# Performance work log

Measured on AMD Instinct MI355X. Metric: run time of the kernel, lower is better.

The kernel has to match this reference:

```python
import jax, jax.numpy as jnp
import numpy as np

T, B, D, H = 512, 256, 256, 256


def setup_inputs() -> dict:
    key = jax.random.key(0)
    ks = jax.random.split(key, 8)
    x = jax.random.normal(ks[0], (T, B, D), dtype=jnp.float32)
    h0 = jax.random.normal(ks[1], (1, B, H), dtype=jnp.float32)
    c0 = jax.random.normal(ks[2], (1, B, H), dtype=jnp.float32)
    W_ih = jax.random.normal(ks[3], (4 * H, D), dtype=jnp.float32) / np.sqrt(D)
    W_hh = jax.random.normal(ks[4], (4 * H, H), dtype=jnp.float32) / np.sqrt(H)
    b_ih = jnp.zeros((4 * H,), dtype=jnp.float32)
    b_hh = jnp.zeros((4 * H,), dtype=jnp.float32)
    done = jax.random.randint(ks[5], (T, B), 0, 2, dtype=jnp.int32)
    return {"x": x, "h0": h0, "c0": c0, "W_ih": W_ih, "W_hh": W_hh,
            "b_ih": b_ih, "b_hh": b_hh, "done": done}


def reference(x, h0, c0, W_ih, W_hh, b_ih, b_hh, done):
    done_f = done.astype(x.dtype)  # [T, B]
    # Precompute input contribution to gates for all timesteps: [T, B, 4H]
    gx = jnp.einsum('tbd,gd->tbg', x, W_ih) + b_ih + b_hh

    def step(carry, inp):
        h, c = carry                      # [B, H] each
        gxt, dt = inp                     # [B, 4H], [B]
        mask = (1.0 - dt)[:, None]        # reset hidden state where done
        h = h * mask
        c = c * mask
        gates = gxt + jnp.einsum('bh,gh->bg', h, W_hh)  # [B, 4H]
        i, f, g, o = jnp.split(gates, 4, axis=-1)       # PyTorch LSTM gate order
        c = jax.nn.sigmoid(f) * c + jax.nn.sigmoid(i) * jnp.tanh(g)
        h = jax.nn.sigmoid(o) * jnp.tanh(c)
        return (h, c), h

    (hT, cT), feats = jax.lax.scan(step, (h0[0], c0[0]), (gx, done_f))
    rnn_feature = feats.reshape(T * B, H)
    return rnn_feature, hT[None], cT[None]
```

## Files before the change

kernel.cpp:

```cpp
#include <hip/hip_runtime.h>
#include <math.h>

#define T_DIM 512
#define B_DIM 256
#define D_DIM 256
#define H_DIM 256
#define G_DIM 1024
#define K_DIM 512
#define NROUNDS 40
#define CHAIN_K 16

typedef __attribute__((ext_vector_type(8))) short short8;
typedef __attribute__((ext_vector_type(4))) float f32x4;

__device__ __forceinline__ unsigned int f2bf(float f) {
    unsigned int b = __float_as_uint(f);
    return (b + 0x7FFFu + ((b >> 16) & 1u)) >> 16;
}
__device__ __forceinline__ unsigned long long pack4(float4 v) {
    const unsigned int lo = (f2bf(v.y) << 16) | f2bf(v.x);
    const unsigned int hi = (f2bf(v.w) << 16) | f2bf(v.z);
    return ((unsigned long long)hi << 32) | lo;
}
__device__ __forceinline__ float sigm(float x) { return 1.0f / (1.0f + __expf(-x)); }
__device__ __forceinline__ float tanh_fast(float x) { return 2.0f / (1.0f + __expf(-2.0f * x)) - 1.0f; }

__device__ __forceinline__ void dma16(const void* g, void* l) {
    __builtin_amdgcn_global_load_lds(
        (const __attribute__((address_space(1))) void*)g,
        (__attribute__((address_space(3))) void*)l, 16, 0, 0);
}

__global__ __launch_bounds__(256) void k_prep_weights(
    const float* __restrict__ W_ih, const float* __restrict__ W_hh,
    const float* __restrict__ b_ih, const float* __restrict__ b_hh,
    unsigned int* __restrict__ Wb, float* __restrict__ bias)
{
    const int idx = blockIdx.x * 256 + threadIdx.x;
    const int jp = idx & 3, l = (idx >> 2) & 63, ks = (idx >> 8) & 15, nt = idx >> 12;
    const int g = nt * 16 + (l & 15);
    const int k0 = ks * 32 + ((l >> 4) << 3) + 2 * jp;
    const float w0 = (k0 < D_DIM) ? W_ih[g * D_DIM + k0] : W_hh[g * H_DIM + (k0 - D_DIM)];
    const float w1 = (k0 + 1 < D_DIM) ? W_ih[g * D_DIM + k0 + 1] : W_hh[g * H_DIM + (k0 + 1 - D_DIM)];
    Wb[idx] = (f2bf(w1) << 16) | f2bf(w0);
    if (idx < G_DIM) bias[idx] = b_ih[idx] + b_hh[idx];
}

__global__ __launch_bounds__(256) void k_prep_wq(
    const float* __restrict__ W_ih, const float* __restrict__ W_hh,
    unsigned long long* __restrict__ Wq)
{
    const int idx = blockIdx.x * 256 + threadIdx.x;
    const int kq = idx >> 10, g = idx & (G_DIM - 1);
    float w[4];
    #pragma unroll
    for (int j = 0; j < 4; ++j) {
        const int k = kq * 4 + j;
        w[j] = (k < D_DIM) ? W_ih[g * D_DIM + k] : W_hh[g * H_DIM + (k - D_DIM)];
    }
    Wq[idx] = pack4((float4){w[0], w[1], w[2], w[3]});
}

__global__ __launch_bounds__(256) void k_prep_ab(
    const float* __restrict__ x, unsigned long long* __restrict__ ab_u64)
{
    const int idx = blockIdx.x * 256 + threadIdx.x;
    const int pos = idx >> 6, ch = idx & 63;
    if (ch >= 32) return;
    const float4 v0 = *(const float4*)(x + (size_t)pos * D_DIM + ch * 8);
    const float4 v1 = *(const float4*)(x + (size_t)pos * D_DIM + ch * 8 + 4);
    ab_u64[(size_t)pos * 128 + ch * 2]     = pack4(v0);
    ab_u64[(size_t)pos * 128 + ch * 2 + 1] = pack4(v1);
}

__global__ __launch_bounds__(256) void k_prefill(
    const float* __restrict__ h0, const int* __restrict__ done,
    unsigned long long* __restrict__ ab_u64)
{
    const int idx = blockIdx.x * 256 + threadIdx.x;
    const int pos = idx >> 5, ch = idx & 31;
    const int d = done[pos];
    if (!d && pos >= B_DIM) return;
    unsigned long long v0 = 0ull, v1 = 0ull;
    if (!d) {
        const float4 a = *(const float4*)(h0 + (size_t)(pos & (B_DIM - 1)) * H_DIM + ch * 8);
        const float4 b = *(const float4*)(h0 + (size_t)(pos & (B_DIM - 1)) * H_DIM + ch * 8 + 4);
        v0 = pack4(a); v1 = pack4(b);
    }
    ab_u64[(size_t)pos * 128 + 64 + ch * 2]     = v0;
    ab_u64[(size_t)pos * 128 + 64 + ch * 2 + 1] = v1;
}

__global__ __launch_bounds__(256) void k_kmap(
    const int* __restrict__ done, int* __restrict__ kmap, int* __restrict__ counts)
{
    __shared__ int lcnt[NROUNDS];
    const int tid = threadIdx.x;
    if (tid < NROUNDS) lcnt[tid] = 0;
    __syncthreads();
    const int t = blockIdx.x, b = tid;
    int kv = t;
    for (int tt = t; tt >= 0; --tt) {
        if (done[tt * B_DIM + b]) { kv = t - tt; break; }
    }
    kmap[t * B_DIM + b] = kv;
    const int bin = kv < NROUNDS ? kv : NROUNDS - 1;
    atomicAdd(&lcnt[bin], 1);
    __syncthreads();
    if (tid < NROUNDS && lcnt[tid] > 0) atomicAdd(&counts[tid], lcnt[tid]);
}

__global__ __launch_bounds__(64) void k_offs(
    const int* __restrict__ counts, int* __restrict__ offs, int* __restrict__ cursor)
{
    if (threadIdx.x == 0) {
        int s = 0;
        for (int i = 0; i < NROUNDS; ++i) { offs[i] = s; s += counts[i]; }
    }
    if (threadIdx.x < NROUNDS) cursor[threadIdx.x] = 0;
}

__global__ __launch_bounds__(256) void k_scatter(
    const int* __restrict__ kmap, const int* __restrict__ offs,
    int* __restrict__ cursor, int* __restrict__ rowlist)
{
    __shared__ int lcnt[NROUNDS];
    __shared__ int gbase[NROUNDS];
    const int tid = threadIdx.x;
    if (tid < NROUNDS) lcnt[tid] = 0;
    __syncthreads();
    const int pos = blockIdx.x * 256 + tid;
    const int kv0 = kmap[pos];
    const int kv = kv0 < NROUNDS ? kv0 : NROUNDS - 1;
    const int lrank = atomicAdd(&lcnt[kv], 1);
    __syncthreads();
    if (tid < NROUNDS && lcnt[tid] > 0) gbase[tid] = atomicAdd(&cursor[tid], lcnt[tid]);
    __syncthreads();
    rowlist[offs[kv] + gbase[kv] + lrank] = pos;
}

__global__ __launch_bounds__(512, 1) void k_round(
    const short* __restrict__ ab, const float* __restrict__ c0,
    const int* __restrict__ done,
    const short* __restrict__ Wb, const float* __restrict__ bias,
    const int* __restrict__ counts, const int* __restrict__ offs,
    const int* __restrict__ rowlist,
    float* __restrict__ out, float* __restrict__ c_buf,
    short* __restrict__ ab_w, int kk)
{
    __shared__ short A_lds[2 * 32 * 512];
    __shared__ float scr[4 * 64 * 36];
    const int nk = counts[kk];
    const int base = offs[kk];
    const int ntiles = (nk + 31) >> 5;

    int cb, rt, rstride;
    if (gridDim.x == 256) {
        const int xcd = blockIdx.x & 7, slot = blockIdx.x >> 3;
        cb = slot & 3;
        rt = xcd * 8 + (slot >> 2);
        rstride = 64;
    } else {
        cb = blockIdx.x & 3;
        rt = blockIdx.x >> 2;
        rstride = gridDim.x >> 2;
    }
    if (rt >= ntiles) return;

    const int tid = threadIdx.x;
    const int w = tid >> 6, l = tid & 63;
    const int lr = l >> 4, lc = l & 15;
    const int q = w & 3, gth = w >> 2;

    const int u_ep = cb * 64 + l;
    const float bI = bias[u_ep], bF = bias[256 + u_ep], bG = bias[512 + u_ep], bO = bias[768 + u_ep];

#define ISSUE_A(PP, bufv)                                                        \
    {                                                                            \
        _Pragma("unroll") for (int rr = 0; rr < 4; ++rr) {                       \
            const int r_ = w * 4 + rr;                                           \
            dma16(ab + (size_t)PP[rr] * 512 + ((l ^ (r_ & 15)) << 3),            \
                  &A_lds[(bufv) * 16384 + r_ * 512]);                            \
        }                                                                        \
    }
#define LOAD_NEXT(row0v, PP, CP, DN, DS)                                         \
    {                                                                            \
        _Pragma("unroll") for (int j_ = 0; j_ < 4; ++j_) {                       \
            const int gr_ = (row0v) + w * 4 + j_;                                \
            PP[j_] = rowlist[base + (gr_ < nk ? gr_ : nk - 1)];                  \
        }                                                                        \
        _Pragma("unroll") for (int j_ = 0; j_ < 4; ++j_) {                       \
            const int p_ = PP[j_];                                               \
            if (kk > 0) {                                                        \
                CP[j_] = c_buf[(size_t)(p_ - B_DIM) * H_DIM + u_ep];             \
                DN[j_] = 0;                                                      \
            } else {                                                             \
                DN[j_] = done[p_];                                               \
                CP[j_] = c0[(size_t)(p_ & (B_DIM - 1)) * H_DIM + u_ep];          \
            }                                                                    \
            const int sp_ = p_ + B_DIM;                                          \
            DS[j_] = (sp_ < T_DIM * B_DIM) ? done[sp_] : 1;                      \
        }                                                                        \
    }

    int posC[4], dnC[4], dsC[4]; float cpC[4];
    LOAD_NEXT(rt * 32, posC, cpC, dnC, dsC);
    ISSUE_A(posC, 0);
    short8 breg0[16], breg1[16];
    {
        const int nt0 = (2 * gth + 0) * 16 + cb * 4 + q;
        const int nt1 = (2 * gth + 1) * 16 + cb * 4 + q;
        #pragma unroll
        for (int ks = 0; ks < 16; ++ks) {
            breg0[ks] = *(const short8*)(Wb + (((size_t)nt0 * 16 + ks) * 64 + l) * 8);
            breg1[ks] = *(const short8*)(Wb + (((size_t)nt1 * 16 + ks) * 64 + l) * 8);
        }
    }

    int buf = 0;
    for (; rt < ntiles; rt += rstride) {
        const int row0 = rt * 32;

        asm volatile("s_waitcnt vmcnt(0) lgkmcnt(0)" ::: "memory");
        __builtin_amdgcn_sched_barrier(0);
        __builtin_amdgcn_s_barrier();
        __builtin_amdgcn_sched_barrier(0);
        const int rtn = rt + rstride;
        const bool more = (rtn < ntiles);
        int posN[4], dnN[4], dsN[4]; float cpN[4];
        if (more) {
            LOAD_NEXT(rtn * 32, posN, cpN, dnN, dsN);
            ISSUE_A(posN, buf ^ 1);
        }

        f32x4 acc0[2], acc1[2];
        #pragma unroll
        for (int mb = 0; mb < 2; ++mb) { acc0[mb] = (f32x4){0,0,0,0}; acc1[mb] = (f32x4){0,0,0,0}; }
        #pragma unroll
        for (int ks = 0; ks < 16; ++ks) {
            #pragma unroll
            for (int mb = 0; mb < 2; ++mb) {
                const short8 a = *(const short8*)&A_lds[buf * 16384 + (mb * 16 + lc) * 512
                                                       + (((ks * 4 + lr) ^ lc) << 3)];
                acc0[mb] = __builtin_amdgcn_mfma_f32_16x16x32_bf16(a, breg0[ks], acc0[mb], 0, 0, 0);
                acc1[mb] = __builtin_amdgcn_mfma_f32_16x16x32_bf16(a, breg1[ks], acc1[mb], 0, 0, 0);
            }
        }

        #pragma unroll
        for (int mb = 0; mb < 2; ++mb) {
            *(f32x4*)&scr[(((2 * gth + 0) * 64 + q * 16 + lc) * 36) + mb * 16 + lr * 4] = acc0[mb];
            *(f32x4*)&scr[(((2 * gth + 1) * 64 + q * 16 + lc) * 36) + mb * 16 + lr * 4] = acc1[mb];
        }
        asm volatile("s_waitcnt lgkmcnt(0)" ::: "memory");
        __builtin_amdgcn_sched_barrier(0);
        __builtin_amdgcn_s_barrier();
        __builtin_amdgcn_sched_barrier(0);

        const f32x4 vi = *(const f32x4*)&scr[((0 * 64 + l) * 36) + w * 4];
        const f32x4 vf = *(const f32x4*)&scr[((1 * 64 + l) * 36) + w * 4];
        const f32x4 vg = *(const f32x4*)&scr[((2 * 64 + l) * 36) + w * 4];
        const f32x4 vo = *(const f32x4*)&scr[((3 * 64 + l) * 36) + w * 4];
        #pragma unroll
        for (int j = 0; j < 4; ++j) {
            const int gr = row0 + w * 4 + j;
            if (gr < nk) {
                const int pos = posC[j];
                const float cp = dnC[j] ? 0.0f : cpC[j];
                const float si = sigm(vi[j] + bI);
                const float sf = sigm(vf[j] + bF);
                const float tg = tanh_fast(vg[j] + bG);
                const float so = sigm(vo[j] + bO);
                const float cn = sf * cp + si * tg;
                const float hn = so * tanh_fast(cn);
                c_buf[(size_t)pos * H_DIM + u_ep] = cn;
                out[(size_t)pos * H_DIM + u_ep]  = hn;
                if (kk + 1 < CHAIN_K && !dsC[j]) {
                    ab_w[(size_t)(pos + B_DIM) * 512 + 256 + u_ep] = (short)f2bf(hn);
                }
            }
        }

        #pragma unroll
        for (int j = 0; j < 4; ++j) { posC[j] = posN[j]; cpC[j] = cpN[j]; dnC[j] = dnN[j]; dsC[j] = dsN[j]; }
        buf ^= 1;
    }
#undef ISSUE_A
#undef LOAD_NEXT
}

__global__ __launch_bounds__(512, 1) void k_round_legacy(
    const float* __restrict__ x, const float* __restrict__ h0,
    const float* __restrict__ c0, const int* __restrict__ done,
    const short* __restrict__ Wb, const float* __restrict__ bias,
    const int* __restrict__ counts, const int* __restrict__ offs,
    const int* __restrict__ rowlist,
    float* __restrict__ out, float* __restrict__ c_buf, int kk)
{
    __shared__ short A_lds[16 * 4 * 64 * 8];
    __shared__ short B_lds[8][8][64 * 8];
    __shared__ int posr[64];
    const int nk = counts[kk];
    const int base = offs[kk];
    const int tid = threadIdx.x;
    const int w = tid >> 6, l = tid & 63;
    const int lr = l >> 4, lc = l & 15;

    const int u_pw = w * 32 + lc;
    float bI[2], bF[2], bG[2], bO[2];
    #pragma unroll
    for (int uq = 0; uq < 2; ++uq) {
        bI[uq] = bias[u_pw + uq * 16];
        bF[uq] = bias[256 + u_pw + uq * 16];
        bG[uq] = bias[512 + u_pw + uq * 16];
        bO[uq] = bias[768 + u_pw + uq * 16];
    }

#define ISSUE_BL(ksv)                                                           \
    {                                                                           \
        _Pragma("unroll") for (int f = 0; f < 8; ++f) {                         \
            const int nt = (f >> 1) * 16 + w * 2 + (f & 1);                     \
            dma16(Wb + (((size_t)nt * 16 + (ksv)) * 64 + l) * 8, &B_lds[w][f][0]); \
        }                                                                       \
    }

    for (int tile = blockIdx.x; tile * 64 < nk; tile += gridDim.x) {
        const int row0 = tile * 64;
        if (tid < 64)
            posr[tid] = (row0 + tid < nk) ? rowlist[base + row0 + tid] : -1;
        __syncthreads();

        unsigned long long* A_u64 = (unsigned long long*)A_lds;
        #pragma unroll 4
        for (int it = 0; it < 16; ++it) {
            const int qq = it * 512 + tid;
            const int ks = qq >> 9, mb = (qq >> 7) & 3, sl = (qq >> 1) & 63, jq = qq & 1;
            const int r = mb * 16 + (sl & 15);
            const int c = ks * 32 + ((sl >> 4) << 3) + 4 * jq;
            const int pos = posr[r];
            float4 v = {0.f, 0.f, 0.f, 0.f};
            if (pos >= 0) {
                if (c < D_DIM) {
                    v = *(const float4*)(x + (size_t)pos * D_DIM + c);
                } else {
                    const int uu = c - D_DIM;
                    if (kk > 0)          v = *(const float4*)(out + (size_t)(pos - B_DIM) * H_DIM + uu);
                    else if (!done[pos]) v = *(const float4*)(h0 + (size_t)(pos & (B_DIM - 1)) * H_DIM + uu);
                }
            }
            A_u64[qq] = pack4(v);
        }
        __syncthreads();

        f32x4 acc[4][4][2];
        #pragma unroll
        for (int gt = 0; gt < 4; ++gt)
            #pragma unroll
            for (int mb = 0; mb < 4; ++mb)
                #pragma unroll
                for (int uq = 0; uq < 2; ++uq)
                    acc[gt][mb][uq] = (f32x4){0.f, 0.f, 0.f, 0.f};

        ISSUE_BL(0);
        #pragma unroll 1
        for (int ks = 0; ks < 16; ++ks) {
            asm volatile("s_waitcnt vmcnt(0)" ::: "memory");
            short8 b[8];
            #pragma unroll
            for (int f = 0; f < 8; ++f)
                b[f] = *(const short8*)&B_lds[w][f][l * 8];
            asm volatile("s_waitcnt lgkmcnt(0)" ::: "memory");
            __builtin_amdgcn_sched_barrier(0);
            if (ks + 1 < 16) ISSUE_BL(ks + 1);
            #pragma unroll
            for (int mb = 0; mb < 4; ++mb) {
                const short8 a = *(const short8*)&A_lds[((ks * 4 + mb) * 64 + l) * 8];
                #pragma unroll
                for (int f = 0; f < 8; ++f)
                    acc[f >> 1][mb][f & 1] = __builtin_amdgcn_mfma_f32_16x16x32_bf16(
                        a, b[f], acc[f >> 1][mb][f & 1], 0, 0, 0);
            }
        }

        #pragma unroll
        for (int mb = 0; mb < 4; ++mb) {
            #pragma unroll
            for (int uq = 0; uq < 2; ++uq) {
                const int uu = w * 32 + uq * 16 + lc;
                #pragma unroll
                for (int j = 0; j < 4; ++j) {
                    const int gr = row0 + mb * 16 + lr * 4 + j;
                    if (gr < nk) {
                        const int pos = posr[mb * 16 + lr * 4 + j];
                        float cp = 0.0f;
                        if (kk > 0)           cp = c_buf[(size_t)(pos - B_DIM) * H_DIM + uu];
                        else if (!done[pos])  cp = c0[(size_t)(pos & (B_DIM - 1)) * H_DIM + uu];
                        const float si = sigm(acc[0][mb][uq][j] + bI[uq]);
                        const float sf = sigm(acc[1][mb][uq][j] + bF[uq]);
                        const float tg = tanh_fast(acc[2][mb][uq][j] + bG[uq]);
                        const float so = sigm(acc[3][mb][uq][j] + bO[uq]);
                        const float cn = sf * cp + si * tg;
                        const float hn = so * tanh_fast(cn);
                        c_buf[(size_t)pos * H_DIM + uu] = cn;
                        out[(size_t)pos * H_DIM + uu]  = hn;
                    }
                }
            }
        }
        __syncthreads();
    }
#undef ISSUE_BL
}

__global__ __launch_bounds__(1024) void k_finish(
    const float* __restrict__ x, const unsigned long long* __restrict__ Wq,
    const float* __restrict__ bias,
    const int* __restrict__ counts, const int* __restrict__ offs,
    const int* __restrict__ rowlist, const int* __restrict__ kmap,
    float* __restrict__ out, float* __restrict__ c_buf)
{
    __shared__ float abuf[K_DIM];
    __shared__ float dots[G_DIM];
    const int g = threadIdx.x;
    const int nch = counts[CHAIN_K];

    for (int m = blockIdx.x; m < nch; m += gridDim.x) {
        const int pos0 = rowlist[offs[CHAIN_K] + m];
        float c_u = 0.0f;
        if (g < H_DIM) {
            abuf[H_DIM + g] = out[(size_t)(pos0 - B_DIM) * H_DIM + g];
            c_u = c_buf[(size_t)(pos0 - B_DIM) * H_DIM + g];
        }
        int pos = pos0, step = CHAIN_K;
        while (true) {
            if (g < H_DIM) abuf[g] = x[(size_t)pos * D_DIM + g];
            __syncthreads();
            float dot = bias[g];
            #pragma unroll 8
            for (int kq = 0; kq < K_DIM / 4; ++kq) {
                const unsigned long long wq = Wq[(size_t)kq * G_DIM + g];
                const float4 a = *(const float4*)&abuf[kq * 4];
                const unsigned int wlo = (unsigned int)wq;
                const unsigned int whi = (unsigned int)(wq >> 32);
                const float w0 = __uint_as_float(wlo << 16);
                const float w1 = __uint_as_float(wlo & 0xFFFF0000u);
                const float w2 = __uint_as_float(whi << 16);
                const float w3 = __uint_as_float(whi & 0xFFFF0000u);
                dot = fmaf(a.x, w0, dot);
                dot = fmaf(a.y, w1, dot);
                dot = fmaf(a.z, w2, dot);
                dot = fmaf(a.w, w3, dot);
            }
            dots[g] = dot;
            __syncthreads();
            if (g < H_DIM) {
                const float si = sigm(dots[g]);
                const float sf = sigm(dots[H_DIM + g]);
                const float tg = tanh_fast(dots[2 * H_DIM + g]);
                const float so = sigm(dots[3 * H_DIM + g]);
                c_u = sf * c_u + si * tg;
                const float hn = so * tanh_fast(c_u);
                out[(size_t)pos * H_DIM + g]   = hn;
                c_buf[(size_t)pos * H_DIM + g] = c_u;
                abuf[H_DIM + g] = hn;
            }
            pos += B_DIM;
            ++step;
            __syncthreads();
            if (pos >= T_DIM * B_DIM) break;
            if (kmap[pos] != step) break;
        }
        __syncthreads();
    }
}

__global__ __launch_bounds__(256) void k_final(const float* __restrict__ c_buf, float* __restrict__ out)
{
    const size_t i = (size_t)blockIdx.x * 256 + threadIdx.x;
    const size_t featN = (size_t)T_DIM * B_DIM * H_DIM;
    const size_t last  = (size_t)(T_DIM - 1) * B_DIM * H_DIM;
    out[featN + i] = out[last + i];
    out[featN + (size_t)B_DIM * H_DIM + i] = c_buf[last + i];
}

__global__ __launch_bounds__(64) void k_zero(int* __restrict__ counts)
{
    if (threadIdx.x < NROUNDS) counts[threadIdx.x] = 0;
}

extern "C" void kernel_launch(void* const* d_in, const int* in_sizes, int n_in,
                              void* d_out, int out_size, void* d_ws, size_t ws_size,
                              hipStream_t stream)
{
    const float* x    = (const float*)d_in[0];
    const float* h0   = (const float*)d_in[1];
    const float* c0   = (const float*)d_in[2];
    const float* W_ih = (const float*)d_in[3];
    const float* W_hh = (const float*)d_in[4];
    const float* b_ih = (const float*)d_in[5];
    const float* b_hh = (const float*)d_in[6];
    const int*   done = (const int*)d_in[7];
    float* out = (float*)d_out;

    const size_t TB = (size_t)T_DIM * B_DIM;
    char* ws = (char*)d_ws;
    size_t off = 0;
    float* c_buf = (float*)(ws + off);            off += TB * H_DIM * 4;
    unsigned int* Wb = (unsigned int*)(ws + off); off += (size_t)(K_DIM / 2) * G_DIM * 4;
    unsigned long long* Wq = (unsigned long long*)(ws + off); off += (size_t)(K_DIM / 4) * G_DIM * 8;
    float* bias = (float*)(ws + off);             off += (size_t)G_DIM * 4;
    int* kmap    = (int*)(ws + off);              off += TB * 4;
    int* rowlist = (int*)(ws + off);              off += TB * 4;
    int* counts  = (int*)(ws + off);              off += 256;
    int* offs    = (int*)(ws + off);              off += 256;
    int* cursor  = (int*)(ws + off);              off += 256;
    short* ab = (short*)(ws + off);
    const size_t need_ab = off + TB * 512 * 2;
    const bool big = (ws_size >= need_ab);

    k_zero<<<1, 64, 0, stream>>>(counts);
    k_prep_weights<<<1024, 256, 0, stream>>>(W_ih, W_hh, b_ih, b_hh, Wb, bias);
    k_prep_wq<<<512, 256, 0, stream>>>(W_ih, W_hh, Wq);
    if (big) {
        k_prep_ab<<<(int)(TB * 64 / 256), 256, 0, stream>>>(x, (unsigned long long*)ab);
        k_prefill<<<(int)(TB * 32 / 256), 256, 0, stream>>>(h0, done, (unsigned long long*)ab);
    }
    k_kmap<<<T_DIM, 256, 0, stream>>>(done, kmap, counts);
    k_offs<<<1, 64, 0, stream>>>(counts, offs, cursor);
    k_scatter<<<(int)(TB / 256), 256, 0, stream>>>(kmap, offs, cursor, rowlist);

    int est = 70000;
    for (int k = 0; k < CHAIN_K; ++k) {
        if (big) {
            int rgs = (est + 31) / 32;
            if (rgs > 64) rgs = 64;
            if (rgs < 1) rgs = 1;
            k_round<<<4 * rgs, 512, 0, stream>>>((const short*)ab, c0, done, (const short*)Wb,
                                                 bias, counts, offs, rowlist, out, c_buf, ab, k);
        } else {
            int grid = est / 64 + 2;
            if (grid > 256) grid = 256;
            if (grid < 8) grid = 8;
            k_round_legacy<<<grid, 512, 0, stream>>>(x, h0, c0, done, (const short*)Wb, bias,
                                                     counts, offs, rowlist, out, c_buf, k);
        }
        est >>= 1;
    }
    k_finish<<<64, 1024, 0, stream>>>(x, Wq, bias, counts, offs, rowlist, kmap, out, c_buf);
    k_final<<<B_DIM * H_DIM / 256, 256, 0, stream>>>(c_buf, out);
}
```

Baseline: 551.4 us.

## Split k_round gate columns across 8 blocks, deterministic scan-based row bucketing

The round kernel now splits hidden units into 8 column chunks of 32 instead of 4 of 64. Each wave holds a single set of B fragments in registers and the epilogue reads gates from a smaller scratch buffer, with a barrier moved to the end of each tile. Row bucketing replaces global atomics with per-timestep counts, a single-block prefix scan and a deterministic in-block rank. The legacy fallback path and the zeroing kernel are removed. This trades fewer registers and more parallel blocks per row tile for extra A-tile reloads across column blocks and a serial scan kernel.

New measurement: 790.2 us. 43.3% more time.

```diff
diff --git a/kernel.cpp b/kernel.cpp
--- a/kernel.cpp
+++ b/kernel.cpp
@@ -92,7 +92,7 @@
 }
 
 __global__ __launch_bounds__(256) void k_kmap(
-    const int* __restrict__ done, int* __restrict__ kmap, int* __restrict__ counts)
+    const int* __restrict__ done, int* __restrict__ kmap, int* __restrict__ bcnt)
 {
     __shared__ int lcnt[NROUNDS];
     const int tid = threadIdx.x;
@@ -107,36 +107,51 @@
     const int bin = kv < NROUNDS ? kv : NROUNDS - 1;
     atomicAdd(&lcnt[bin], 1);
     __syncthreads();
-    if (tid < NROUNDS && lcnt[tid] > 0) atomicAdd(&counts[tid], lcnt[tid]);
-}
-
-__global__ __launch_bounds__(64) void k_offs(
-    const int* __restrict__ counts, int* __restrict__ offs, int* __restrict__ cursor)
-{
-    if (threadIdx.x == 0) {
+    if (tid < NROUNDS) bcnt[t * NROUNDS + tid] = lcnt[tid];
+}
+
+__global__ __launch_bounds__(512) void k_scan(
+    const int* __restrict__ bcnt, int* __restrict__ boffs,
+    int* __restrict__ counts, int* __restrict__ offs)
+{
+    __shared__ int tmp[512];
+    __shared__ int tot[NROUNDS];
+    const int t = threadIdx.x;
+    for (int bin = 0; bin < NROUNDS; ++bin) {
+        const int v = bcnt[t * NROUNDS + bin];
+        tmp[t] = v;
+        __syncthreads();
+        for (int d = 1; d < 512; d <<= 1) {
+            const int add = (t >= d) ? tmp[t - d] : 0;
+            __syncthreads();
+            tmp[t] += add;
+            __syncthreads();
+        }
+        boffs[t * NROUNDS + bin] = tmp[t] - v;
+        if (t == 511) tot[bin] = tmp[511];
+        __syncthreads();
+    }
+    if (t == 0) {
         int s = 0;
-        for (int i = 0; i < NROUNDS; ++i) { offs[i] = s; s += counts[i]; }
-    }
-    if (threadIdx.x < NROUNDS) cursor[threadIdx.x] = 0;
+        for (int i = 0; i < NROUNDS; ++i) { counts[i] = tot[i]; offs[i] = s; s += tot[i]; }
+    }
 }
 
 __global__ __launch_bounds__(256) void k_scatter(
     const int* __restrict__ kmap, const int* __restrict__ offs,
-    int* __restrict__ cursor, int* __restrict__ rowlist)
-{
-    __shared__ int lcnt[NROUNDS];
-    __shared__ int gbase[NROUNDS];
-    const int tid = threadIdx.x;
-    if (tid < NROUNDS) lcnt[tid] = 0;
+    const int* __restrict__ boffs, int* __restrict__ rowlist)
+{
+    __shared__ int bins[256];
+    const int t = blockIdx.x, tid = threadIdx.x;
+    const int pos = t * 256 + tid;
+    const int kv = kmap[pos];
+    const int bin = kv < NROUNDS ? kv : NROUNDS - 1;
+    bins[tid] = bin;
     __syncthreads();
-    const int pos = blockIdx.x * 256 + tid;
-    const int kv0 = kmap[pos];
-    const int kv = kv0 < NROUNDS ? kv0 : NROUNDS - 1;
-    const int lrank = atomicAdd(&lcnt[kv], 1);
-    __syncthreads();
-    if (tid < NROUNDS && lcnt[tid] > 0) gbase[tid] = atomicAdd(&cursor[tid], lcnt[tid]);
-    __syncthreads();
-    rowlist[offs[kv] + gbase[kv] + lrank] = pos;
+    int rank = 0;
+    for (int i = 0; i < 256; ++i)
+        rank += (i < tid && bins[i] == bin) ? 1 : 0;
+    rowlist[offs[bin] + boffs[t * NROUNDS + bin] + rank] = pos;
 }
 
 __global__ __launch_bounds__(512, 1) void k_round(
@@ -149,7 +164,7 @@
     short* __restrict__ ab_w, int kk)
 {
     __shared__ short A_lds[2 * 32 * 512];
-    __shared__ float scr[4 * 64 * 36];
+    __shared__ float scr[4 * 32 * 33];
     const int nk = counts[kk];
     const int base = offs[kk];
     const int ntiles = (nk + 31) >> 5;
@@ -157,39 +172,44 @@
     int cb, rt, rstride;
     if (gridDim.x == 256) {
         const int xcd = blockIdx.x & 7, slot = blockIdx.x >> 3;
-        cb = slot & 3;
-        rt = xcd * 8 + (slot >> 2);
-        rstride = 64;
+        cb = slot & 7;
+        rt = xcd * 4 + (slot >> 3);
+        rstride = 32;
     } else {
-        cb = blockIdx.x & 3;
-        rt = blockIdx.x >> 2;
-        rstride = gridDim.x >> 2;
+        cb = blockIdx.x & 7;
+        rt = blockIdx.x >> 3;
+        rstride = gridDim.x >> 3;
     }
     if (rt >= ntiles) return;
 
     const int tid = threadIdx.x;
     const int w = tid >> 6, l = tid & 63;
     const int lr = l >> 4, lc = l & 15;
-    const int q = w & 3, gth = w >> 2;
-
-    const int u_ep = cb * 64 + l;
+
+    const int u_loc = tid & 31;
+    const int u_ep = cb * 32 + u_loc;
+    const int rbase = (tid >> 5) * 2;
     const float bI = bias[u_ep], bF = bias[256 + u_ep], bG = bias[512 + u_ep], bO = bias[768 + u_ep];
 
-#define ISSUE_A(PP, bufv)                                                        \
+#define ISSUE_A(row0v, bufv)                                                     \
     {                                                                            \
         _Pragma("unroll") for (int rr = 0; rr < 4; ++rr) {                       \
             const int r_ = w * 4 + rr;                                           \
-            dma16(ab + (size_t)PP[rr] * 512 + ((l ^ (r_ & 15)) << 3),            \
-                  &A_lds[(bufv) * 16384 + r_ * 512]);                            \
+            const int gr_ = (row0v) + r_;                                        \
+            if (gr_ < nk) {                                                      \
+                const int p_ = rowlist[base + gr_];                              \
+                dma16(ab + (size_t)p_ * 512 + ((l ^ (r_ & 15)) << 3),            \
+                      &A_lds[(bufv) * 16384 + r_ * 512]);                        \
+            }                                                                    \
         }                                                                        \
     }
 #define LOAD_NEXT(row0v, PP, CP, DN, DS)                                         \
     {                                                                            \
-        _Pragma("unroll") for (int j_ = 0; j_ < 4; ++j_) {                       \
-            const int gr_ = (row0v) + w * 4 + j_;                                \
+        _Pragma("unroll") for (int j_ = 0; j_ < 2; ++j_) {                       \
+            const int gr_ = (row0v) + rbase + j_;                                \
             PP[j_] = rowlist[base + (gr_ < nk ? gr_ : nk - 1)];                  \
         }                                                                        \
-        _Pragma("unroll") for (int j_ = 0; j_ < 4; ++j_) {                       \
+        _Pragma("unroll") for (int j_ = 0; j_ < 2; ++j_) {                       \
             const int p_ = PP[j_];                                               \
             if (kk > 0) {                                                        \
                 CP[j_] = c_buf[(size_t)(p_ - B_DIM) * H_DIM + u_ep];             \
@@ -203,213 +223,96 @@
         }                                                                        \
     }
 
-    int posC[4], dnC[4], dsC[4]; float cpC[4];
+    int posC[2], dnC[2], dsC[2]; float cpC[2];
     LOAD_NEXT(rt * 32, posC, cpC, dnC, dsC);
-    ISSUE_A(posC, 0);
-    short8 breg0[16], breg1[16];
+    ISSUE_A(rt * 32, 0);
+    short8 breg[16];
     {
-        const int nt0 = (2 * gth + 0) * 16 + cb * 4 + q;
-        const int nt1 = (2 * gth + 1) * 16 + cb * 4 + q;
+        const int nt = (w >> 1) * 16 + cb * 2 + (w & 1);
         #pragma unroll
-        for (int ks = 0; ks < 16; ++ks) {
-            breg0[ks] = *(const short8*)(Wb + (((size_t)nt0 * 16 + ks) * 64 + l) * 8);
-            breg1[ks] = *(const short8*)(Wb + (((size_t)nt1 * 16 + ks) * 64 + l) * 8);
-        }
-    }
+        for (int ks = 0; ks < 16; ++ks)
+            breg[ks] = *(const short8*)(Wb + (((size_t)nt * 16 + ks) * 64 + l) * 8);
+        #pragma unroll
+        for (int ks = 0; ks < 16; ++ks)
+            asm volatile("" : "+v"(breg[ks]));
+    }
+    asm volatile("s_waitcnt vmcnt(0) lgkmcnt(0)" ::: "memory");
+    __builtin_amdgcn_sched_barrier(0);
+    __builtin_amdgcn_s_barrier();
+    __builtin_amdgcn_sched_barrier(0);
 
     int buf = 0;
     for (; rt < ntiles; rt += rstride) {
         const int row0 = rt * 32;
-
-        asm volatile("s_waitcnt vmcnt(0) lgkmcnt(0)" ::: "memory");
-        __builtin_amdgcn_sched_barrier(0);
-        __builtin_amdgcn_s_barrier();
-        __builtin_amdgcn_sched_barrier(0);
         const int rtn = rt + rstride;
         const bool more = (rtn < ntiles);
-        int posN[4], dnN[4], dsN[4]; float cpN[4];
+
+        int posN[2], dnN[2], dsN[2]; float cpN[2];
         if (more) {
             LOAD_NEXT(rtn * 32, posN, cpN, dnN, dsN);
-            ISSUE_A(posN, buf ^ 1);
-        }
-
-        f32x4 acc0[2], acc1[2];
-        #pragma unroll
-        for (int mb = 0; mb < 2; ++mb) { acc0[mb] = (f32x4){0,0,0,0}; acc1[mb] = (f32x4){0,0,0,0}; }
+            ISSUE_A(rtn * 32, buf ^ 1);
+        }
+
+        f32x4 acc[2];
+        acc[0] = (f32x4){0, 0, 0, 0};
+        acc[1] = (f32x4){0, 0, 0, 0};
         #pragma unroll
         for (int ks = 0; ks < 16; ++ks) {
             #pragma unroll
             for (int mb = 0; mb < 2; ++mb) {
                 const short8 a = *(const short8*)&A_lds[buf * 16384 + (mb * 16 + lc) * 512
                                                        + (((ks * 4 + lr) ^ lc) << 3)];
-                acc0[mb] = __builtin_amdgcn_mfma_f32_16x16x32_bf16(a, breg0[ks], acc0[mb], 0, 0, 0);
-                acc1[mb] = __builtin_amdgcn_mfma_f32_16x16x32_bf16(a, breg1[ks], acc1[mb], 0, 0, 0);
+                acc[mb] = __builtin_amdgcn_mfma_f32_16x16x32_bf16(a, breg[ks], acc[mb], 0, 0, 0);
             }
         }
 
-        #pragma unroll
-        for (int mb = 0; mb < 2; ++mb) {
-            *(f32x4*)&scr[(((2 * gth + 0) * 64 + q * 16 + lc) * 36) + mb * 16 + lr * 4] = acc0[mb];
-            *(f32x4*)&scr[(((2 * gth + 1) * 64 + q * 16 + lc) * 36) + mb * 16 + lr * 4] = acc1[mb];
+        {
+            const int gidx = (w >> 1) * 32 + (w & 1) * 16 + lc;
+            *(f32x4*)&scr[gidx * 33 + 0 * 16 + lr * 4] = acc[0];
+            *(f32x4*)&scr[gidx * 33 + 1 * 16 + lr * 4] = acc[1];
         }
         asm volatile("s_waitcnt lgkmcnt(0)" ::: "memory");
         __builtin_amdgcn_sched_barrier(0);
         __builtin_amdgcn_s_barrier();
         __builtin_amdgcn_sched_barrier(0);
 
-        const f32x4 vi = *(const f32x4*)&scr[((0 * 64 + l) * 36) + w * 4];
-        const f32x4 vf = *(const f32x4*)&scr[((1 * 64 + l) * 36) + w * 4];
-        const f32x4 vg = *(const f32x4*)&scr[((2 * 64 + l) * 36) + w * 4];
-        const f32x4 vo = *(const f32x4*)&scr[((3 * 64 + l) * 36) + w * 4];
         #pragma unroll
-        for (int j = 0; j < 4; ++j) {
-            const int gr = row0 + w * 4 + j;
+        for (int j = 0; j < 2; ++j) {
+            const int gr = row0 + rbase + j;
             if (gr < nk) {
+                const int r = rbase + j;
+                const float vi = scr[(0 * 32 + u_loc) * 33 + r];
+                const float vf = scr[(1 * 32 + u_loc) * 33 + r];
+                const float vg = scr[(2 * 32 + u_loc) * 33 + r];
+                const float vo = scr[(3 * 32 + u_loc) * 33 + r];
                 const int pos = posC[j];
                 const float cp = dnC[j] ? 0.0f : cpC[j];
-                const float si = sigm(vi[j] + bI);
-                const float sf = sigm(vf[j] + bF);
-                const float tg = tanh_fast(vg[j] + bG);
-                const float so = sigm(vo[j] + bO);
+                const float si = sigm(vi + bI);
+                const float sf = sigm(vf + bF);
+                const float tg = tanh_fast(vg + bG);
+                const float so = sigm(vo + bO);
                 const float cn = sf * cp + si * tg;
                 const float hn = so * tanh_fast(cn);
                 c_buf[(size_t)pos * H_DIM + u_ep] = cn;
                 out[(size_t)pos * H_DIM + u_ep]  = hn;
-                if (kk + 1 < CHAIN_K && !dsC[j]) {
+                if (kk + 1 < CHAIN_K && !dsC[j])
                     ab_w[(size_t)(pos + B_DIM) * 512 + 256 + u_ep] = (short)f2bf(hn);
-                }
             }
         }
 
-        #pragma unroll
-        for (int j = 0; j < 4; ++j) { posC[j] = posN[j]; cpC[j] = cpN[j]; dnC[j] = dnN[j]; dsC[j] = dsN[j]; }
+        asm volatile("s_waitcnt vmcnt(4) lgkmcnt(0)" ::: "memory");
+        __builtin_amdgcn_sched_barrier(0);
+        __builtin_amdgcn_s_barrier();
+        __builtin_amdgcn_sched_barrier(0);
+
+        posC[0] = posN[0]; posC[1] = posN[1];
+        cpC[0] = cpN[0];  cpC[1] = cpN[1];
+        dnC[0] = dnN[0];  dnC[1] = dnN[1];
+        dsC[0] = dsN[0];  dsC[1] = dsN[1];
         buf ^= 1;
     }
 #undef ISSUE_A
 #undef LOAD_NEXT
-}
-
-__global__ __launch_bounds__(512, 1) void k_round_legacy(
-    const float* __restrict__ x, const float* __restrict__ h0,
-    const float* __restrict__ c0, const int* __restrict__ done,
-    const short* __restrict__ Wb, const float* __restrict__ bias,
-    const int* __restrict__ counts, const int* __restrict__ offs,
-    const int* __restrict__ rowlist,
-    float* __restrict__ out, float* __restrict__ c_buf, int kk)
-{
-    __shared__ short A_lds[16 * 4 * 64 * 8];
-    __shared__ short B_lds[8][8][64 * 8];
-    __shared__ int posr[64];
-    const int nk = counts[kk];
-    const int base = offs[kk];
-    const int tid = threadIdx.x;
-    const int w = tid >> 6, l = tid & 63;
-    const int lr = l >> 4, lc = l & 15;
-
-    const int u_pw = w * 32 + lc;
-    float bI[2], bF[2], bG[2], bO[2];
-    #pragma unroll
-    for (int uq = 0; uq < 2; ++uq) {
-        bI[uq] = bias[u_pw + uq * 16];
-        bF[uq] = bias[256 + u_pw + uq * 16];
-        bG[uq] = bias[512 + u_pw + uq * 16];
-        bO[uq] = bias[768 + u_pw + uq * 16];
-    }
-
-#define ISSUE_BL(ksv)                                                           \
-    {                                                                           \
-        _Pragma("unroll") for (int f = 0; f < 8; ++f) {                         \
-            const int nt = (f >> 1) * 16 + w * 2 + (f & 1);                     \
-            dma16(Wb + (((size_t)nt * 16 + (ksv)) * 64 + l) * 8, &B_lds[w][f][0]); \
-        }                                                                       \
-    }
-
-    for (int tile = blockIdx.x; tile * 64 < nk; tile += gridDim.x) {
-        const int row0 = tile * 64;
-        if (tid < 64)
-            posr[tid] = (row0 + tid < nk) ? rowlist[base + row0 + tid] : -1;
-        __syncthreads();
-
-        unsigned long long* A_u64 = (unsigned long long*)A_lds;
-        #pragma unroll 4
-        for (int it = 0; it < 16; ++it) {
-            const int qq = it * 512 + tid;
-            const int ks = qq >> 9, mb = (qq >> 7) & 3, sl = (qq >> 1) & 63, jq = qq & 1;
-            const int r = mb * 16 + (sl & 15);
-            const int c = ks * 32 + ((sl >> 4) << 3) + 4 * jq;
-            const int pos = posr[r];
-            float4 v = {0.f, 0.f, 0.f, 0.f};
-            if (pos >= 0) {
-                if (c < D_DIM) {
-                    v = *(const float4*)(x + (size_t)pos * D_DIM + c);
-                } else {
-                    const int uu = c - D_DIM;
-                    if (kk > 0)          v = *(const float4*)(out + (size_t)(pos - B_DIM) * H_DIM + uu);
-                    else if (!done[pos]) v = *(const float4*)(h0 + (size_t)(pos & (B_DIM - 1)) * H_DIM + uu);
-                }
-            }
-            A_u64[qq] = pack4(v);
-        }
-        __syncthreads();
-
-        f32x4 acc[4][4][2];
-        #pragma unroll
-        for (int gt = 0; gt < 4; ++gt)
-            #pragma unroll
-            for (int mb = 0; mb < 4; ++mb)
-                #pragma unroll
-                for (int uq = 0; uq < 2; ++uq)
-                    acc[gt][mb][uq] = (f32x4){0.f, 0.f, 0.f, 0.f};
-
-        ISSUE_BL(0);
-        #pragma unroll 1
-        for (int ks = 0; ks < 16; ++ks) {
-            asm volatile("s_waitcnt vmcnt(0)" ::: "memory");
-            short8 b[8];
-            #pragma unroll
-            for (int f = 0; f < 8; ++f)
-                b[f] = *(const short8*)&B_lds[w][f][l * 8];
-            asm volatile("s_waitcnt lgkmcnt(0)" ::: "memory");
-            __builtin_amdgcn_sched_barrier(0);
-            if (ks + 1 < 16) ISSUE_BL(ks + 1);
-            #pragma unroll
-            for (int mb = 0; mb < 4; ++mb) {
-                const short8 a = *(const short8*)&A_lds[((ks * 4 + mb) * 64 + l) * 8];
-                #pragma unroll
-                for (int f = 0; f < 8; ++f)
-                    acc[f >> 1][mb][f & 1] = __builtin_amdgcn_mfma_f32_16x16x32_bf16(
-                        a, b[f], acc[f >> 1][mb][f & 1], 0, 0, 0);
-            }
-        }
-
-        #pragma unroll
-        for (int mb = 0; mb < 4; ++mb) {
-            #pragma unroll
-            for (int uq = 0; uq < 2; ++uq) {
-                const int uu = w * 32 + uq * 16 + lc;
-                #pragma unroll
-                for (int j = 0; j < 4; ++j) {
-                    const int gr = row0 + mb * 16 + lr * 4 + j;
-                    if (gr < nk) {
-                        const int pos = posr[mb * 16 + lr * 4 + j];
-                        float cp = 0.0f;
-                        if (kk > 0)           cp = c_buf[(size_t)(pos - B_DIM) * H_DIM + uu];
-                        else if (!done[pos])  cp = c0[(size_t)(pos & (B_DIM - 1)) * H_DIM + uu];
-                        const float si = sigm(acc[0][mb][uq][j] + bI[uq]);
-                        const float sf = sigm(acc[1][mb][uq][j] + bF[uq]);
-                        const float tg = tanh_fast(acc[2][mb][uq][j] + bG[uq]);
-                        const float so = sigm(acc[3][mb][uq][j] + bO[uq]);
-                        const float cn = sf * cp + si * tg;
-                        const float hn = so * tanh_fast(cn);
-                        c_buf[(size_t)pos * H_DIM + uu] = cn;
-                        out[(size_t)pos * H_DIM + uu]  = hn;
-                    }
-                }
-            }
-        }
-        __syncthreads();
-    }
-#undef ISSUE_BL
 }
 
 __global__ __launch_bounds__(1024) void k_finish(
@@ -483,11 +386,6 @@
     out[featN + (size_t)B_DIM * H_DIM + i] = c_buf[last + i];
 }
 
-__global__ __launch_bounds__(64) void k_zero(int* __restrict__ counts)
-{
-    if (threadIdx.x < NROUNDS) counts[threadIdx.x] = 0;
-}
-
 extern "C" void kernel_launch(void* const* d_in, const int* in_sizes, int n_in,
                               void* d_out, int out_size, void* d_ws, size_t ws_size,
                               hipStream_t stream)
@@ -513,37 +411,25 @@
     int* rowlist = (int*)(ws + off);              off += TB * 4;
     int* counts  = (int*)(ws + off);              off += 256;
     int* offs    = (int*)(ws + off);              off += 256;
-    int* cursor  = (int*)(ws + off);              off += 256;
-    short* ab = (short*)(ws + off);
-    const size_t need_ab = off + TB * 512 * 2;
-    const bool big = (ws_size >= need_ab);
-
-    k_zero<<<1, 64, 0, stream>>>(counts);
+    int* bcnt    = (int*)(ws + off);              off += (size_t)T_DIM * NROUNDS * 4;
+    int* boffs   = (int*)(ws + off);              off += (size_t)T_DIM * NROUNDS * 4;
+    short* ab = (short*)(ws + off);               off += TB * 512 * 2;
+
     k_prep_weights<<<1024, 256, 0, stream>>>(W_ih, W_hh, b_ih, b_hh, Wb, bias);
     k_prep_wq<<<512, 256, 0, stream>>>(W_ih, W_hh, Wq);
-    if (big) {
-        k_prep_ab<<<(int)(TB * 64 / 256), 256, 0, stream>>>(x, (unsigned long long*)ab);
-        k_prefill<<<(int)(TB * 32 / 256), 256, 0, stream>>>(h0, done, (unsigned long long*)ab);
-    }
-    k_kmap<<<T_DIM, 256, 0, stream>>>(done, kmap, counts);
-    k_offs<<<1, 64, 0, stream>>>(counts, offs, cursor);
-    k_scatter<<<(int)(TB / 256), 256, 0, stream>>>(kmap, offs, cursor, rowlist);
+    k_prep_ab<<<(int)(TB * 64 / 256), 256, 0, stream>>>(x, (unsigned long long*)ab);
+    k_prefill<<<(int)(TB * 32 / 256), 256, 0, stream>>>(h0, done, (unsigned long long*)ab);
+    k_kmap<<<T_DIM, 256, 0, stream>>>(done, kmap, bcnt);
+    k_scan<<<1, 512, 0, stream>>>(bcnt, boffs, counts, offs);
+    k_scatter<<<(int)(TB / 256), 256, 0, stream>>>(kmap, offs, boffs, rowlist);
 
     int est = 70000;
     for (int k = 0; k < CHAIN_K; ++k) {
-        if (big) {
-            int rgs = (est + 31) / 32;
-            if (rgs > 64) rgs = 64;
-            if (rgs < 1) rgs = 1;
-            k_round<<<4 * rgs, 512, 0, stream>>>((const short*)ab, c0, done, (const short*)Wb,
-                                                 bias, counts, offs, rowlist, out, c_buf, ab, k);
-        } else {
-            int grid = est / 64 + 2;
-            if (grid > 256) grid = 256;
-            if (grid < 8) grid = 8;
-            k_round_legacy<<<grid, 512, 0, stream>>>(x, h0, c0, done, (const short*)Wb, bias,
-                                                     counts, offs, rowlist, out, c_buf, k);
-        }
+        int rch = (est + 31) / 32;
+        if (rch > 32) rch = 32;
+        if (rch < 1) rch = 1;
+        k_round<<<8 * rch, 512, 0, stream>>>((const short*)ab, c0, done, (const short*)Wb,
+                                             bias, counts, offs, rowlist, out, c_buf, ab, k);
         est >>= 1;
     }
     k_finish<<<64, 1024, 0, stream>>>(x, Wq, bias, counts, offs, rowlist, kmap, out, c_buf);
```
